# Kernel tuning notes

Hardware: AMD Instinct MI355X
Metric: run time of the kernel (lower is better)

The kernel has to match this reference:

```python
import jax, jax.numpy as jnp
import numpy as np

B = 32768
D_VIS, D_LANG, D_STATE = 256, 128, 128
D_MODEL, N_EXP, TOP_K = 512, 8, 2
D_IN = D_VIS + D_LANG + D_STATE
EPS = 1e-5

def _gelu(x):
    # torch nn.GELU default = exact erf form
    return jax.nn.gelu(x, approximate=False)

def _ln(x, g, b):
    mu = x.mean(-1, keepdims=True)
    var = ((x - mu) ** 2).mean(-1, keepdims=True)
    return (x - mu) / jnp.sqrt(var + EPS) * g + b

def setup_inputs() -> dict:
    key = jax.random.key(0)
    ks = jax.random.split(key, 16)
    f32 = jnp.float32
    def w(k, shape, fan_in):
        return jax.random.normal(k, shape, dtype=f32) * (1.0 / np.sqrt(fan_in))
    return {
        "vis":   jax.random.normal(ks[0], (B, D_VIS), dtype=f32),
        "lang":  jax.random.normal(ks[1], (B, D_LANG), dtype=f32),
        "state": jax.random.normal(ks[2], (B, D_STATE), dtype=f32),
        # fusion: Linear(D_IN, D_MODEL) + LayerNorm + GELU
        "Wf": w(ks[3], (D_IN, D_MODEL), D_IN),
        "bf": jnp.zeros((D_MODEL,), f32),
        "gf": jnp.ones((D_MODEL,), f32),
        "betaf": jnp.zeros((D_MODEL,), f32),
        # gate (bias-free); random instead of torch's zeros-init so routing is non-degenerate
        "Wg": w(ks[4], (D_MODEL, N_EXP), D_MODEL),
        # stacked expert params: d -> 2d -> d -> d, residual LayerNorm
        "W1": w(ks[5], (N_EXP, D_MODEL, 2 * D_MODEL), D_MODEL),
        "b1": jnp.zeros((N_EXP, 2 * D_MODEL), f32),
        "W2": w(ks[6], (N_EXP, 2 * D_MODEL, D_MODEL), 2 * D_MODEL),
        "b2": jnp.zeros((N_EXP, D_MODEL), f32),
        "W3": w(ks[7], (N_EXP, D_MODEL, D_MODEL), D_MODEL),
        "b3": jnp.zeros((N_EXP, D_MODEL), f32),
        "ge": jnp.ones((N_EXP, D_MODEL), f32),
        "be": jnp.zeros((N_EXP, D_MODEL), f32),
    }

def reference(vis, lang, state, Wf, bf, gf, betaf, Wg, W1, b1, W2, b2, W3, b3, ge, be):
    # fusion projection  [B, D_IN] -> [B, D_MODEL]
    x = _gelu(_ln(jnp.concatenate([vis, lang, state], axis=-1) @ Wf + bf, gf, betaf))
    logits = x @ Wg                              # [B, E]
    all_probs = jax.nn.softmax(logits, axis=-1)  # [B, E]
    top_vals, top_idx = jax.lax.top_k(logits, TOP_K)   # [B, K]
    top_w = jax.nn.softmax(top_vals, axis=-1)          # [B, K]
    # per-(token, expert) combine weight: sum_k top_w[b,k] * [top_idx[b,k]==e]
    onehot = jax.nn.one_hot(top_idx, N_EXP, dtype=x.dtype)   # [B, K, E]
    combine = (onehot * top_w[..., None]).sum(axis=1)        # [B, E]
    out = jnp.zeros_like(x)
    for e in range(N_EXP):  # small fixed expert count; dense compute, sparse combine
        h = _gelu(x @ W1[e] + b1[e])
        h = _gelu(h @ W2[e] + b2[e])
        h = h @ W3[e] + b3[e]
        y = _ln(x + h, ge[e], be[e])            # Expert: ln(x + net(x))
        out = out + combine[:, e:e + 1] * y
    # load-balancing aux loss (counts carry no gradient, as in torch scatter_add of ones)
    counts = onehot.sum(axis=(0, 1))            # [E]
    f_i = counts / (B * TOP_K)
    lb_loss = N_EXP * jnp.sum(f_i * all_probs.mean(axis=0))
    return out, lb_loss
```

## Files before the change

### kernel.cpp

```cpp
#include <hip/hip_runtime.h>
#include <math.h>

typedef __bf16     bf16x8 __attribute__((ext_vector_type(8)));
typedef _Float16   f16x8  __attribute__((ext_vector_type(8)));
typedef float      f32x4  __attribute__((ext_vector_type(4)));
typedef unsigned short u16x8 __attribute__((ext_vector_type(8)));

#define DEVI __device__ __forceinline__
constexpr int B_TOK = 32768;
constexpr int MAXT  = 520;
constexpr int NBLK  = B_TOK / 16;

DEVI unsigned short f2bf(float f){
  unsigned int u = __builtin_bit_cast(unsigned int, f);
  u += 0x7fffu + ((u >> 16) & 1u);
  return (unsigned short)(u >> 16);
}
DEVI float bf2f(unsigned short b){
  return __builtin_bit_cast(float, (unsigned int)b << 16);
}
DEVI float gelu_fast(float x){
  float z = fabsf(x) * 0.70710678118654752f;
  float t = __builtin_amdgcn_rcpf(1.f + 0.3275911f * z);
  float p = t*(0.254829592f + t*(-0.284496736f + t*(1.421413741f + t*(-1.453152027f + t*1.061405429f))));
  float e = __expf(-z * z);
  float erfz = 1.f - p * e;
  float s = copysignf(erfz, x);
  return 0.5f * x * (1.f + s);
}
DEVI void load16_lds(const void* g, void* l){
  __builtin_amdgcn_global_load_lds(
      (const __attribute__((address_space(1))) unsigned int*)g,
      (__attribute__((address_space(3))) unsigned int*)l, 16, 0, 0);
}
DEVI float wredsum(float v){
#pragma unroll
  for (int off = 32; off > 0; off >>= 1) v += __shfl_xor(v, off, 64);
  return v;
}

__global__ void transpose_cast_bf16_k(const float* __restrict__ src, unsigned short* __restrict__ dst,
                                      int R, int C){
  __shared__ float tile[32][33];
  size_t base = (size_t)blockIdx.z * R * C;
  int c0 = blockIdx.x * 32, r0 = blockIdx.y * 32;
  for (int i = threadIdx.y; i < 32; i += 8)
    tile[i][threadIdx.x] = src[base + (size_t)(r0 + i) * C + c0 + threadIdx.x];
  __syncthreads();
  for (int i = threadIdx.y; i < 32; i += 8)
    dst[base + (size_t)(c0 + i) * R + r0 + threadIdx.x] = f2bf(tile[threadIdx.x][i]);
}

__global__ void transpose_split_f16_k(const float* __restrict__ src, unsigned short* __restrict__ dh,
                                      unsigned short* __restrict__ dl, int R, int C){
  __shared__ float tile[32][33];
  int c0 = blockIdx.x * 32, r0 = blockIdx.y * 32;
  for (int i = threadIdx.y; i < 32; i += 8)
    tile[i][threadIdx.x] = src[(size_t)(r0 + i) * C + c0 + threadIdx.x];
  __syncthreads();
  for (int i = threadIdx.y; i < 32; i += 8){
    float f = tile[threadIdx.x][i];
    _Float16 h = (_Float16)f;
    _Float16 l = (_Float16)(f - (float)h);
    size_t o = (size_t)(c0 + i) * R + r0 + threadIdx.x;
    dh[o] = __builtin_bit_cast(unsigned short, h);
    dl[o] = __builtin_bit_cast(unsigned short, l);
  }
}

__global__ __launch_bounds__(256, 2) void gemm_fusion_f16split(
    const float* __restrict__ vis, const float* __restrict__ lang, const float* __restrict__ state,
    const unsigned short* __restrict__ Wh, const unsigned short* __restrict__ Wl,
    const float* __restrict__ bias, float* __restrict__ Xpre)
{
  constexpr int K = 512, N = 512;
  __shared__ alignas(16) unsigned short smemF[32768];
  unsigned short* AhS = smemF;
  unsigned short* AlS = smemF + 8192;
  unsigned short* BhS = smemF + 16384;
  unsigned short* BlS = smemF + 24576;
  const int tid = threadIdx.x;
  const int row_s = tid >> 3, col_s = (tid & 7) * 8;
  const int swz = (row_s & 7) << 3;
  const unsigned short *pbh[4], *pbl[4];
  int arow[4];
#pragma unroll
  for (int i = 0; i < 4; ++i){
    arow[i] = blockIdx.x * 128 + i * 32 + row_s;
    size_t br = (size_t)(blockIdx.y * 128 + i * 32 + row_s) * K + (col_s ^ swz);
    pbh[i] = Wh + br; pbl[i] = Wl + br;
  }
  const int w = tid >> 6, lane = tid & 63;
  const int wr = (w >> 1) * 64, wc = (w & 1) * 64;
  const int lm = lane & 15, lk8 = (lane >> 4) * 8;
  const int fxor = (lm & 7) << 3;
  f32x4 acc[4][4] = {};
  for (int k0 = 0; k0 < K; k0 += 64){
#pragma unroll
    for (int i = 0; i < 4; ++i){
      load16_lds(pbh[i] + k0, &BhS[i*2048 + tid*8]);
      load16_lds(pbl[i] + k0, &BlS[i*2048 + tid*8]);
    }
    int col = k0 + col_s;
#pragma unroll
    for (int i = 0; i < 4; ++i){
      const float* src;
      if (col < 256)      src = vis   + (size_t)arow[i] * 256 + col;
      else if (col < 384) src = lang  + (size_t)arow[i] * 128 + (col - 256);
      else                src = state + (size_t)arow[i] * 128 + (col - 384);
      float4 a = *(const float4*)src, b = *(const float4*)(src + 4);
      float f[8] = {a.x, a.y, a.z, a.w, b.x, b.y, b.z, b.w};
      u16x8 hh, ll;
#pragma unroll
      for (int j = 0; j < 8; ++j){
        _Float16 h = (_Float16)f[j];
        _Float16 l = (_Float16)(f[j] - (float)h);
        hh[j] = __builtin_bit_cast(unsigned short, h);
        ll[j] = __builtin_bit_cast(unsigned short, l);
      }
      *(u16x8*)&AhS[i*2048 + row_s*64 + (col_s ^ swz)] = hh;
      *(u16x8*)&AlS[i*2048 + row_s*64 + (col_s ^ swz)] = ll;
    }
    __syncthreads();
#pragma unroll
    for (int kk = 0; kk < 64; kk += 32){
      f16x8 fah[4], fal[4], fbh[4], fbl[4];
#pragma unroll
      for (int m = 0; m < 4; ++m){
        int ro = (wr + m*16 + lm) * 64 + ((kk + lk8) ^ fxor);
        fah[m] = *(const f16x8*)&AhS[ro];
        fal[m] = *(const f16x8*)&AlS[ro];
      }
#pragma unroll
      for (int n = 0; n < 4; ++n){
        int ro = (wc + n*16 + lm) * 64 + ((kk + lk8) ^ fxor);
        fbh[n] = *(const f16x8*)&BhS[ro];
        fbl[n] = *(const f16x8*)&BlS[ro];
      }
#pragma unroll
      for (int m = 0; m < 4; ++m)
#pragma unroll
        for (int n = 0; n < 4; ++n){
          acc[m][n] = __builtin_amdgcn_mfma_f32_16x16x32_f16(fah[m], fbh[n], acc[m][n], 0, 0, 0);
          acc[m][n] = __builtin_amdgcn_mfma_f32_16x16x32_f16(fal[m], fbh[n], acc[m][n], 0, 0, 0);
          acc[m][n] = __builtin_amdgcn_mfma_f32_16x16x32_f16(fah[m], fbl[n], acc[m][n], 0, 0, 0);
        }
    }
    __syncthreads();
  }
  float* Cs = (float*)smemF;
  const int lk4 = (lane >> 4) * 4;
#pragma unroll
  for (int n = 0; n < 4; ++n){
    float bv = bias[blockIdx.y * 128 + wc + n*16 + lm];
#pragma unroll
    for (int m = 0; m < 4; ++m)
#pragma unroll
      for (int r = 0; r < 4; ++r){
        int rr = wr + m*16 + lk4 + r;
        Cs[rr * 128 + ((wc + n*16 + lm) ^ ((rr & 7) << 2))] = acc[m][n][r] + bv;
      }
  }
  __syncthreads();
#pragma unroll
  for (int j = 0; j < 16; ++j){
    int r = j*8 + (tid >> 5), c = (tid & 31) * 4;
    float4 v = *(const float4*)&Cs[r*128 + (c ^ ((r & 7) << 2))];
    *(float4*)&Xpre[(size_t)(blockIdx.x*128 + r) * N + blockIdx.y*128 + c] = v;
  }
}

template<int K, int N, bool GATHER, bool GELU_ACT, bool GLOBAL_ROW>
__global__ __launch_bounds__(256, 2) void egemm_k(
    const unsigned short* __restrict__ A, const int* __restrict__ rowlist,
    const int* __restrict__ cnt, const int* __restrict__ nTilesP,
    const int* __restrict__ tileE, const int* __restrict__ tileR0, int chunkBase,
    const unsigned short* __restrict__ W, const float* __restrict__ bias,
    unsigned short* __restrict__ Cout)
{
  const int t = chunkBase + blockIdx.y;
  if (t >= nTilesP[0]) return;
  const int e = tileE[t], r0 = tileR0[t];
  int rows = cnt[e] - r0; rows = rows > 128 ? 128 : rows;
  __shared__ alignas(16) unsigned short smem[16384];
  unsigned short* As = smem;
  unsigned short* Bs = smem + 8192;
  const int tid = threadIdx.x;
  const int row_s = tid >> 3, col_s = (tid & 7) * 8;
  const int swz = (row_s & 7) << 3;
  const unsigned short *pa[4], *pb[4];
#pragma unroll
  for (int i = 0; i < 4; ++i){
    int ir = i * 32 + row_s;
    size_t arow;
    if (GATHER){
      int rr = ir < rows ? ir : rows - 1;
      arow = (size_t)rowlist[(size_t)e * B_TOK + r0 + rr];
    } else {
      arow = (size_t)blockIdx.y * 128 + ir;
    }
    pa[i] = A + arow * K + (col_s ^ swz);
    pb[i] = W + (size_t)e * ((size_t)N * K) + (size_t)(blockIdx.x * 128 + ir) * K + (col_s ^ swz);
  }
  const int w = tid >> 6, lane = tid & 63;
  const int wr = (w >> 1) * 64, wc = (w & 1) * 64;
  const int lm = lane & 15, lk8 = (lane >> 4) * 8;
  const int fxor = (lm & 7) << 3;
  f32x4 acc[4][4] = {};
  for (int k0 = 0; k0 < K; k0 += 64){
#pragma unroll
    for (int i = 0; i < 4; ++i) load16_lds(pa[i] + k0, &As[i*2048 + tid*8]);
#pragma unroll
    for (int i = 0; i < 4; ++i) load16_lds(pb[i] + k0, &Bs[i*2048 + tid*8]);
    __syncthreads();
#pragma unroll
    for (int kk = 0; kk < 64; kk += 32){
      bf16x8 a[4], b[4];
#pragma unroll
      for (int m = 0; m < 4; ++m)
        a[m] = *(const bf16x8*)&As[(wr + m*16 + lm)*64 + ((kk + lk8) ^ fxor)];
#pragma unroll
      for (int n = 0; n < 4; ++n)
        b[n] = *(const bf16x8*)&Bs[(wc + n*16 + lm)*64 + ((kk + lk8) ^ fxor)];
#pragma unroll
      for (int m = 0; m < 4; ++m)
#pragma unroll
        for (int n = 0; n < 4; ++n)
          acc[m][n] = __builtin_amdgcn_mfma_f32_16x16x32_bf16(a[m], b[n], acc[m][n], 0, 0, 0);
    }
    __syncthreads();
  }
  unsigned short* Cs = smem;
  const int lk4 = (lane >> 4) * 4;
#pragma unroll
  for (int n = 0; n < 4; ++n){
    float bv = bias[(size_t)e * N + blockIdx.x * 128 + wc + n*16 + lm];
#pragma unroll
    for (int m = 0; m < 4; ++m)
#pragma unroll
      for (int r = 0; r < 4; ++r){
        float v = acc[m][n][r] + bv;
        if (GELU_ACT) v = gelu_fast(v);
        int rr = wr + m*16 + lk4 + r;
        Cs[rr * 128 + ((wc + n*16 + lm) ^ ((rr & 7) << 3))] = f2bf(v);
      }
  }
  __syncthreads();
  const size_t outTile = GLOBAL_ROW ? (size_t)t * 128 : (size_t)blockIdx.y * 128;
#pragma unroll
  for (int j = 0; j < 8; ++j){
    int r = j*16 + (tid >> 4), c = (tid & 15) * 8;
    if (r < rows){
      u16x8 v = *(const u16x8*)&Cs[r*128 + (c ^ ((r & 7) << 3))];
      *(u16x8*)&Cout[(outTile + r) * N + blockIdx.x*128 + c] = v;
    }
  }
}

__global__ __launch_bounds__(256) void ln_gelu_gate_k(
    const float* __restrict__ Xpre, const float* __restrict__ gf,
    const float* __restrict__ betaf, const float* __restrict__ Wg,
    unsigned short* __restrict__ Xbf, int* __restrict__ PK,
    int* __restrict__ BlockCnt, float* __restrict__ BlockProbs)
{
  __shared__ float s_probs[8];
  __shared__ int s_cnt[8];
  __shared__ int s_pk[16];
  __shared__ float s_w[16];
  const int tid = threadIdx.x, wv = tid >> 6, lane = tid & 63;
  if (tid < 8){ s_probs[tid] = 0.f; s_cnt[tid] = 0; }
  __syncthreads();
  float gg[8], bb[8], wg[8][8];
  {
    const float4* gp = (const float4*)(gf + lane * 8);
    const float4* bp = (const float4*)(betaf + lane * 8);
    float4 g0 = gp[0], g1 = gp[1], c0 = bp[0], c1 = bp[1];
    gg[0]=g0.x; gg[1]=g0.y; gg[2]=g0.z; gg[3]=g0.w; gg[4]=g1.x; gg[5]=g1.y; gg[6]=g1.z; gg[7]=g1.w;
    bb[0]=c0.x; bb[1]=c0.y; bb[2]=c0.z; bb[3]=c0.w; bb[4]=c1.x; bb[5]=c1.y; bb[6]=c1.z; bb[7]=c1.w;
#pragma unroll
    for (int j = 0; j < 8; ++j){
      const float4* wrow = (const float4*)(Wg + (size_t)(lane * 8 + j) * 8);
      float4 w0 = wrow[0], w1 = wrow[1];
      wg[j][0]=w0.x; wg[j][1]=w0.y; wg[j][2]=w0.z; wg[j][3]=w0.w;
      wg[j][4]=w1.x; wg[j][5]=w1.y; wg[j][6]=w1.z; wg[j][7]=w1.w;
    }
  }
  float4 vv[4][2];
#pragma unroll
  for (int it = 0; it < 4; ++it){
    const int row = blockIdx.x * 16 + wv * 4 + it;
    const float* xp = Xpre + (size_t)row * 512 + lane * 8;
    vv[it][0] = *(const float4*)xp;
    vv[it][1] = *(const float4*)(xp + 4);
  }
#pragma unroll
  for (int it = 0; it < 4; ++it){
    const int tloc = wv * 4 + it;
    const int row = blockIdx.x * 16 + tloc;
    float v[8] = {vv[it][0].x, vv[it][0].y, vv[it][0].z, vv[it][0].w,
                  vv[it][1].x, vv[it][1].y, vv[it][1].z, vv[it][1].w};
    float s1 = 0.f, s2 = 0.f;
#pragma unroll
    for (int j = 0; j < 8; ++j){ s1 += v[j]; s2 += v[j]*v[j]; }
    {
      float sel = (lane & 1) ? s1 : s2;
      float r = __shfl_xor(sel, 1, 64);
      float tt = ((lane & 1) ? s2 : s1) + r;
#pragma unroll
      for (int off = 2; off < 64; off <<= 1) tt += __shfl_xor(tt, off, 64);
      float other = __shfl_xor(tt, 1, 64);
      s1 = (lane & 1) ? other : tt;
      s2 = (lane & 1) ? tt : other;
    }
    const float mu  = s1 * (1.f / 512.f);
    const float var = s2 * (1.f / 512.f) - mu * mu;
    const float inv = 1.f / sqrtf(var + 1e-5f);
    float o[8];
#pragma unroll
    for (int j = 0; j < 8; ++j)
      o[j] = gelu_fast((v[j] - mu) * inv * gg[j] + bb[j]);
    u16x8 ob;
#pragma unroll
    for (int j = 0; j < 8; ++j) ob[j] = f2bf(o[j]);
    *(u16x8*)(Xbf + (size_t)row * 512 + lane * 8) = ob;
    float acc[8] = {0.f,0.f,0.f,0.f,0.f,0.f,0.f,0.f};
#pragma unroll
    for (int j = 0; j < 8; ++j)
#pragma unroll
      for (int e = 0; e < 8; ++e) acc[e] += o[j] * wg[j][e];
    float v4[4], v2[2], v1f;
#pragma unroll
    for (int i = 0; i < 4; ++i){
      float sel = (lane & 1) ? acc[i] : acc[i+4];
      float r = __shfl_xor(sel, 1, 64);
      v4[i] = ((lane & 1) ? acc[i+4] : acc[i]) + r;
    }
#pragma unroll
    for (int i = 0; i < 2; ++i){
      float sel = (lane & 2) ? v4[i] : v4[i+2];
      float r = __shfl_xor(sel, 2, 64);
      v2[i] = ((lane & 2) ? v4[i+2] : v4[i]) + r;
    }
    {
      float sel = (lane & 4) ? v2[0] : v2[1];
      float r = __shfl_xor(sel, 4, 64);
      v1f = ((lane & 4) ? v2[1] : v2[0]) + r;
    }
#pragma unroll
    for (int off = 8; off < 64; off <<= 1) v1f += __shfl_xor(v1f, off, 64);
    float lg[8];
#pragma unroll
    for (int e = 0; e < 8; ++e){
      int src = (lane & 56) | ((e >> 2) & 1) | (((e >> 1) & 1) << 1) | ((e & 1) << 2);
      lg[e] = __shfl(v1f, src, 64);
    }
    float mx = lg[0];
#pragma unroll
    for (int e = 1; e < 8; ++e) mx = fmaxf(mx, lg[e]);
    float pe[8], ps = 0.f;
#pragma unroll
    for (int e = 0; e < 8; ++e){ pe[e] = __expf(lg[e] - mx); ps += pe[e]; }
    float invp = 1.f / ps;
    int i1 = 0;
#pragma unroll
    for (int e = 1; e < 8; ++e) if (lg[e] > lg[i1]) i1 = e;
    int i2 = (i1 == 0) ? 1 : 0;
#pragma unroll
    for (int e = 0; e < 8; ++e) if (e != i1 && lg[e] > lg[i2]) i2 = e;
    float wA = 1.f / (1.f + __expf(lg[i2] - lg[i1]));
    if (lane == 0){
#pragma unroll
      for (int e = 0; e < 8; ++e) atomicAdd(&s_probs[e], pe[e] * invp);
      int r0 = atomicAdd(&s_cnt[i1], 1);
      int r1 = atomicAdd(&s_cnt[i2], 1);
      s_pk[tloc] = i1 | (r0 << 3) | (i2 << 8) | (r1 << 16);
      s_w[tloc] = wA;
    }
  }
  __syncthreads();
  if (tid < 8){
    BlockCnt[blockIdx.x * 8 + tid] = s_cnt[tid];
    BlockProbs[blockIdx.x * 8 + tid] = s_probs[tid];
  }
  if (tid < 16){
    int t = blockIdx.x * 16 + tid;
    PK[2*t]   = s_pk[tid];
    PK[2*t+1] = __builtin_bit_cast(int, s_w[tid]);
  }
}

__global__ __launch_bounds__(256) void scan_k(
    const int* __restrict__ BlockCnt, const float* __restrict__ BlockProbs,
    int* __restrict__ BlockBase, int* __restrict__ CNT, int* __restrict__ nTiles,
    int* __restrict__ tileE, int* __restrict__ tileR0, int* __restrict__ rowBase,
    float* __restrict__ lbOut)
{
  __shared__ int sScan[256];
  __shared__ float sF[256];
  __shared__ int sTot[8];
  __shared__ float sProbTot[8];
  const int tid = threadIdx.x;
  for (int e = 0; e < 8; ++e){
    int local[8]; int sum = 0;
#pragma unroll
    for (int j = 0; j < 8; ++j){ local[j] = BlockCnt[(tid*8 + j)*8 + e]; sum += local[j]; }
    float fsum = 0.f;
#pragma unroll
    for (int j = 0; j < 8; ++j) fsum += BlockProbs[(tid*8 + j)*8 + e];
    sScan[tid] = sum; sF[tid] = fsum;
    __syncthreads();
    for (int off = 1; off < 256; off <<= 1){
      int add = (tid >= off) ? sScan[tid - off] : 0;
      __syncthreads();
      sScan[tid] += add;
      __syncthreads();
    }
    for (int off = 128; off > 0; off >>= 1){
      if (tid < off) sF[tid] += sF[tid + off];
      __syncthreads();
    }
    int base = (tid == 0) ? 0 : sScan[tid - 1];
    int run = base;
#pragma unroll
    for (int j = 0; j < 8; ++j){ BlockBase[(tid*8 + j)*8 + e] = run; run += local[j]; }
    if (tid == 0){ sTot[e] = sScan[255]; sProbTot[e] = sF[0]; }
    __syncthreads();
  }
  if (tid == 0){
    int t = 0;
    for (int e = 0; e < 8; ++e){
      int c = sTot[e]; c = c < 0 ? 0 : (c > B_TOK ? B_TOK : c);
      CNT[e] = c;
      rowBase[e] = t * 128;
      for (int r = 0; r < c; r += 128){ tileE[t] = e; tileR0[t] = r; ++t; }
    }
    nTiles[0] = t;
    for (int i = t; i < MAXT; ++i){ tileE[i] = 0; tileR0[i] = 0; }
    float acc = 0.f;
    for (int e = 0; e < 8; ++e)
      acc += ((float)sTot[e] / (float)(B_TOK * 2)) * (sProbTot[e] / (float)B_TOK);
    lbOut[0] = 8.f * acc;
  }
}

__global__ __launch_bounds__(256) void place_k(
    const int* __restrict__ PK, const int* __restrict__ BlockBase,
    int* __restrict__ rowlist, int* __restrict__ TS, float* __restrict__ TW)
{
  const int t = blockIdx.x * 256 + threadIdx.x;
  int pk = PK[2*t];
  float w0 = __builtin_bit_cast(float, PK[2*t+1]);
  int e0 = pk & 7, r0 = (pk >> 3) & 31;
  int e1 = (pk >> 8) & 7, r1 = (pk >> 16) & 31;
  int blk = t >> 4;
  int p0 = BlockBase[blk*8 + e0] + r0;
  int p1 = BlockBase[blk*8 + e1] + r1;
  rowlist[(size_t)e0 * B_TOK + p0] = t;
  rowlist[(size_t)e1 * B_TOK + p1] = t;
  TS[2*t]   = (e0 << 15) | p0;  TW[2*t]   = w0;
  TS[2*t+1] = (e1 << 15) | p1;  TW[2*t+1] = 1.f - w0;
}

__global__ __launch_bounds__(256) void combine_k(
    const unsigned short* __restrict__ Xbf, const unsigned short* __restrict__ H3F,
    const int* __restrict__ TS, const float* __restrict__ TW,
    const int* __restrict__ rowBase, const float* __restrict__ ge,
    const float* __restrict__ be, float* __restrict__ out)
{
  const int tok = blockIdx.x * 4 + (threadIdx.x >> 6);
  const int lane = threadIdx.x & 63;
  u16x8 xb = *(const u16x8*)(Xbf + (size_t)tok * 512 + lane * 8);
  float x[8];
#pragma unroll
  for (int j = 0; j < 8; ++j) x[j] = bf2f(xb[j]);
  float o[8] = {0.f,0.f,0.f,0.f,0.f,0.f,0.f,0.f};
#pragma unroll
  for (int kslot = 0; kslot < 2; ++kslot){
    int sl = TS[tok*2 + kslot];
    float wgt = TW[tok*2 + kslot];
    int e = sl >> 15, p = sl & 32767;
    size_t hrow = (size_t)(rowBase[e] + p);
    u16x8 hb = *(const u16x8*)(H3F + hrow * 512 + lane * 8);
    float s[8];
#pragma unroll
    for (int j = 0; j < 8; ++j) s[j] = x[j] + bf2f(hb[j]);
    float sm = 0.f;
#pragma unroll
    for (int j = 0; j < 8; ++j) sm += s[j];
    sm = wredsum(sm);
    float mu = sm * (1.f / 512.f);
    float q = 0.f;
#pragma unroll
    for (int j = 0; j < 8; ++j){ float d = s[j] - mu; q += d * d; }
    q = wredsum(q);
    float inv = 1.f / sqrtf(q * (1.f / 512.f) + 1e-5f);
    const float4* gp = (const float4*)(ge + (size_t)e * 512 + lane * 8);
    const float4* bp = (const float4*)(be + (size_t)e * 512 + lane * 8);
    float4 g0 = gp[0], g1 = gp[1], c0 = bp[0], c1 = bp[1];
    float gg[8] = {g0.x,g0.y,g0.z,g0.w,g1.x,g1.y,g1.z,g1.w};
    float bb[8] = {c0.x,c0.y,c0.z,c0.w,c1.x,c1.y,c1.z,c1.w};
#pragma unroll
    for (int j = 0; j < 8; ++j)
      o[j] += wgt * ((s[j]-mu)*inv*gg[j] + bb[j]);
  }
  float* op = out + (size_t)tok * 512 + lane * 8;
  *(float4*)op       = make_float4(o[0], o[1], o[2], o[3]);
  *(float4*)(op + 4) = make_float4(o[4], o[5], o[6], o[7]);
}

extern "C" void kernel_launch(void* const* d_in, const int* in_sizes, int n_in,
                              void* d_out, int out_size, void* d_ws, size_t ws_size,
                              hipStream_t stream)
{
  (void)in_sizes; (void)n_in; (void)out_size;
  const float* vis   = (const float*)d_in[0];
  const float* lang  = (const float*)d_in[1];
  const float* state = (const float*)d_in[2];
  const float* Wf    = (const float*)d_in[3];
  const float* bf    = (const float*)d_in[4];
  const float* gf    = (const float*)d_in[5];
  const float* betaf = (const float*)d_in[6];
  const float* Wg    = (const float*)d_in[7];
  const float* W1    = (const float*)d_in[8];
  const float* b1    = (const float*)d_in[9];
  const float* W2    = (const float*)d_in[10];
  const float* b2    = (const float*)d_in[11];
  const float* W3    = (const float*)d_in[12];
  const float* b3    = (const float*)d_in[13];
  const float* ge    = (const float*)d_in[14];
  const float* be    = (const float*)d_in[15];

  char* ws = (char*)d_ws;
  size_t off = 0;
  auto alloc = [&](size_t n){ size_t o = off; off += (n + 255) & ~(size_t)255; return o; };

  unsigned short* WFH  = (unsigned short*)(ws + alloc((size_t)512*512*2));
  unsigned short* WFL  = (unsigned short*)(ws + alloc((size_t)512*512*2));
  unsigned short* W1T  = (unsigned short*)(ws + alloc((size_t)8*1024*512*2));
  unsigned short* W2T  = (unsigned short*)(ws + alloc((size_t)8*512*1024*2));
  unsigned short* W3T  = (unsigned short*)(ws + alloc((size_t)8*512*512*2));
  unsigned short* XBF  = (unsigned short*)(ws + alloc((size_t)B_TOK*512*2));
  int*            RLIST= (int*)(ws + alloc((size_t)8*B_TOK*4));
  int*            TS   = (int*)(ws + alloc((size_t)B_TOK*2*4));
  float*          TW   = (float*)(ws + alloc((size_t)B_TOK*2*4));
  int*            PK   = (int*)(ws + alloc((size_t)B_TOK*2*4));
  int*            BCNT = (int*)(ws + alloc((size_t)NBLK*8*4));
  float*          BPROB= (float*)(ws + alloc((size_t)NBLK*8*4));
  int*            BBASE= (int*)(ws + alloc((size_t)NBLK*8*4));
  int*            CNT  = (int*)(ws + alloc(64));
  int*            NT   = (int*)(ws + alloc(64));
  int*            RB   = (int*)(ws + alloc(64));
  int*            TE   = (int*)(ws + alloc(MAXT*4));
  int*            TR   = (int*)(ws + alloc(MAXT*4));
  unsigned short* H3F  = (unsigned short*)(ws + alloc((size_t)MAXT*128*512*2));

  const size_t perTile = (size_t)128*1024*2 + (size_t)128*512*2;
  size_t remain = (ws_size > off) ? (ws_size - off) : 0;
  int tch, nch;
  size_t need2 = (size_t)260 * perTile, need4 = (size_t)B_TOK*512*4;
  if (remain >= need2 && need2 >= need4){ tch = 260; nch = 2; }
  else { tch = 130; nch = 4; }
  size_t regB = alloc(need2 > need4 ? (nch == 2 ? need2 : need4) : need4);
  float*          XPRE = (float*)(ws + regB);
  unsigned short* H1   = (unsigned short*)(ws + regB);
  unsigned short* H2   = H1 + (size_t)tch*128*1024;

  transpose_split_f16_k<<<dim3(16,16,1), dim3(32,8), 0, stream>>>(Wf, WFH, WFL, 512, 512);
  transpose_cast_bf16_k<<<dim3(32,16,8), dim3(32,8), 0, stream>>>(W1, W1T, 512, 1024);
  transpose_cast_bf16_k<<<dim3(16,32,8), dim3(32,8), 0, stream>>>(W2, W2T, 1024, 512);
  transpose_cast_bf16_k<<<dim3(16,16,8), dim3(32,8), 0, stream>>>(W3, W3T, 512, 512);
  gemm_fusion_f16split<<<dim3(256,4), 256, 0, stream>>>(vis, lang, state, WFH, WFL, bf, XPRE);
  ln_gelu_gate_k<<<NBLK, 256, 0, stream>>>(XPRE, gf, betaf, Wg, XBF, PK, BCNT, BPROB);
  scan_k<<<1, 256, 0, stream>>>(BCNT, BPROB, BBASE, CNT, NT, TE, TR, RB,
                                ((float*)d_out) + (size_t)B_TOK*512);
  place_k<<<B_TOK/256, 256, 0, stream>>>(PK, BBASE, RLIST, TS, TW);

  for (int c = 0; c < nch; ++c){
    int cb = c * tch;
    egemm_k<512, 1024, true,  true,  false><<<dim3(8, tch), 256, 0, stream>>>(
        XBF, RLIST, CNT, NT, TE, TR, cb, W1T, b1, H1);
    egemm_k<1024, 512, false, true,  false><<<dim3(4, tch), 256, 0, stream>>>(
        H1,  RLIST, CNT, NT, TE, TR, cb, W2T, b2, H2);
    egemm_k<512,  512, false, false, true ><<<dim3(4, tch), 256, 0, stream>>>(
        H2,  RLIST, CNT, NT, TE, TR, cb, W3T, b3, H3F);
  }
  combine_k<<<B_TOK/4, 256, 0, stream>>>(XBF, H3F, TS, TW, RB, ge, be, (float*)d_out);
}
```

Measured before the change: 546.9 us.

## Remap expert GEMM grid to XCD-grouped tiles and parallelize routing scan

The expert GEMM launches become 1D grids. Block index modulo 8 picks a contiguous group of row tiles, so that blocks landing on the same XCD (the hardware assigns workgroups round-robin across the 8 XCDs) share the A rows and expert weights in their L2. The single-block scan kernel now scans all 8 experts in one pass instead of looping serially, and fills the tile tables in parallel. The gains depend on the XCD dispatch assumption, and the padded grid adds some early-exit blocks.

```diff
diff --git a/kernel.cpp b/kernel.cpp
--- a/kernel.cpp
+++ b/kernel.cpp
@@ -170,15 +170,21 @@
   }
 }
 
-template<int K, int N, bool GATHER, bool GELU_ACT, bool GLOBAL_ROW>
+template<int K, int N, int NT, bool GATHER, bool GELU_ACT, bool GLOBAL_ROW>
 __global__ __launch_bounds__(256, 2) void egemm_k(
     const unsigned short* __restrict__ A, const int* __restrict__ rowlist,
     const int* __restrict__ cnt, const int* __restrict__ nTilesP,
-    const int* __restrict__ tileE, const int* __restrict__ tileR0, int chunkBase,
+    const int* __restrict__ tileE, const int* __restrict__ tileR0,
+    int chunkBase, int chunkTiles, int tpg,
     const unsigned short* __restrict__ W, const float* __restrict__ bias,
     unsigned short* __restrict__ Cout)
 {
-  const int t = chunkBase + blockIdx.y;
+  const int g = blockIdx.x & 7;
+  const int j = blockIdx.x >> 3;
+  const int tloc = g * tpg + j / NT;
+  const int ntile = j % NT;
+  if (tloc >= chunkTiles) return;
+  const int t = chunkBase + tloc;
   if (t >= nTilesP[0]) return;
   const int e = tileE[t], r0 = tileR0[t];
   int rows = cnt[e] - r0; rows = rows > 128 ? 128 : rows;
@@ -197,10 +203,10 @@
       int rr = ir < rows ? ir : rows - 1;
       arow = (size_t)rowlist[(size_t)e * B_TOK + r0 + rr];
     } else {
-      arow = (size_t)blockIdx.y * 128 + ir;
+      arow = (size_t)tloc * 128 + ir;
     }
     pa[i] = A + arow * K + (col_s ^ swz);
-    pb[i] = W + (size_t)e * ((size_t)N * K) + (size_t)(blockIdx.x * 128 + ir) * K + (col_s ^ swz);
+    pb[i] = W + (size_t)e * ((size_t)N * K) + (size_t)(ntile * 128 + ir) * K + (col_s ^ swz);
   }
   const int w = tid >> 6, lane = tid & 63;
   const int wr = (w >> 1) * 64, wc = (w & 1) * 64;
@@ -234,7 +240,7 @@
   const int lk4 = (lane >> 4) * 4;
 #pragma unroll
   for (int n = 0; n < 4; ++n){
-    float bv = bias[(size_t)e * N + blockIdx.x * 128 + wc + n*16 + lm];
+    float bv = bias[(size_t)e * N + ntile * 128 + wc + n*16 + lm];
 #pragma unroll
     for (int m = 0; m < 4; ++m)
 #pragma unroll
@@ -246,13 +252,13 @@
       }
   }
   __syncthreads();
-  const size_t outTile = GLOBAL_ROW ? (size_t)t * 128 : (size_t)blockIdx.y * 128;
-#pragma unroll
-  for (int j = 0; j < 8; ++j){
-    int r = j*16 + (tid >> 4), c = (tid & 15) * 8;
+  const size_t outTile = GLOBAL_ROW ? (size_t)t * 128 : (size_t)tloc * 128;
+#pragma unroll
+  for (int jj = 0; jj < 8; ++jj){
+    int r = jj*16 + (tid >> 4), c = (tid & 15) * 8;
     if (r < rows){
       u16x8 v = *(const u16x8*)&Cs[r*128 + (c ^ ((r & 7) << 3))];
-      *(u16x8*)&Cout[(outTile + r) * N + blockIdx.x*128 + c] = v;
+      *(u16x8*)&Cout[(outTile + r) * N + ntile*128 + c] = v;
     }
   }
 }
@@ -395,51 +401,77 @@
     int* __restrict__ tileE, int* __restrict__ tileR0, int* __restrict__ rowBase,
     float* __restrict__ lbOut)
 {
-  __shared__ int sScan[256];
-  __shared__ float sF[256];
+  __shared__ int sS[8][256];
+  __shared__ float sF[8][256];
   __shared__ int sTot[8];
   __shared__ float sProbTot[8];
+  __shared__ int sTileBase[9];
   const int tid = threadIdx.x;
-  for (int e = 0; e < 8; ++e){
-    int local[8]; int sum = 0;
-#pragma unroll
-    for (int j = 0; j < 8; ++j){ local[j] = BlockCnt[(tid*8 + j)*8 + e]; sum += local[j]; }
-    float fsum = 0.f;
-#pragma unroll
-    for (int j = 0; j < 8; ++j) fsum += BlockProbs[(tid*8 + j)*8 + e];
-    sScan[tid] = sum; sF[tid] = fsum;
+  int local[8][8];
+  int sum[8] = {0,0,0,0,0,0,0,0};
+  float fsum[8] = {0.f,0.f,0.f,0.f,0.f,0.f,0.f,0.f};
+#pragma unroll
+  for (int jb = 0; jb < 8; ++jb){
+    int blk = tid * 8 + jb;
+#pragma unroll
+    for (int e = 0; e < 8; ++e){
+      int c = BlockCnt[blk*8 + e];
+      local[jb][e] = c;
+      sum[e] += c;
+      fsum[e] += BlockProbs[blk*8 + e];
+    }
+  }
+#pragma unroll
+  for (int e = 0; e < 8; ++e){ sS[e][tid] = sum[e]; sF[e][tid] = fsum[e]; }
+  __syncthreads();
+  for (int off = 1; off < 256; off <<= 1){
+    int add[8];
+#pragma unroll
+    for (int e = 0; e < 8; ++e) add[e] = (tid >= off) ? sS[e][tid - off] : 0;
     __syncthreads();
-    for (int off = 1; off < 256; off <<= 1){
-      int add = (tid >= off) ? sScan[tid - off] : 0;
-      __syncthreads();
-      sScan[tid] += add;
-      __syncthreads();
-    }
-    for (int off = 128; off > 0; off >>= 1){
-      if (tid < off) sF[tid] += sF[tid + off];
-      __syncthreads();
-    }
-    int base = (tid == 0) ? 0 : sScan[tid - 1];
-    int run = base;
-#pragma unroll
-    for (int j = 0; j < 8; ++j){ BlockBase[(tid*8 + j)*8 + e] = run; run += local[j]; }
-    if (tid == 0){ sTot[e] = sScan[255]; sProbTot[e] = sF[0]; }
+#pragma unroll
+    for (int e = 0; e < 8; ++e) sS[e][tid] += add[e];
     __syncthreads();
+  }
+  for (int off = 128; off > 0; off >>= 1){
+    if (tid < off)
+#pragma unroll
+      for (int e = 0; e < 8; ++e) sF[e][tid] += sF[e][tid + off];
+    __syncthreads();
+  }
+  int base[8];
+#pragma unroll
+  for (int e = 0; e < 8; ++e) base[e] = (tid == 0) ? 0 : sS[e][tid-1];
+#pragma unroll
+  for (int jb = 0; jb < 8; ++jb){
+    int blk = tid * 8 + jb;
+#pragma unroll
+    for (int e = 0; e < 8; ++e){ BlockBase[blk*8 + e] = base[e]; base[e] += local[jb][e]; }
   }
   if (tid == 0){
     int t = 0;
+    float acc = 0.f;
     for (int e = 0; e < 8; ++e){
-      int c = sTot[e]; c = c < 0 ? 0 : (c > B_TOK ? B_TOK : c);
+      int c = sS[e][255]; c = c < 0 ? 0 : (c > B_TOK ? B_TOK : c);
+      sTot[e] = c;
       CNT[e] = c;
+      sTileBase[e] = t;
       rowBase[e] = t * 128;
-      for (int r = 0; r < c; r += 128){ tileE[t] = e; tileR0[t] = r; ++t; }
-    }
+      t += (c + 127) >> 7;
+      acc += ((float)c / (float)(B_TOK * 2)) * (sF[e][0] / (float)B_TOK);
+    }
+    sTileBase[8] = t;
     nTiles[0] = t;
-    for (int i = t; i < MAXT; ++i){ tileE[i] = 0; tileR0[i] = 0; }
-    float acc = 0.f;
-    for (int e = 0; e < 8; ++e)
-      acc += ((float)sTot[e] / (float)(B_TOK * 2)) * (sProbTot[e] / (float)B_TOK);
     lbOut[0] = 8.f * acc;
+  }
+  __syncthreads();
+  const int ntot = sTileBase[8];
+  for (int i = tid; i < MAXT; i += 256){
+    int e = 0;
+#pragma unroll
+    for (int k = 1; k <= 8; ++k) if (i >= sTileBase[k]) e = k;
+    if (i < ntot){ tileE[i] = e; tileR0[i] = (i - sTileBase[e]) * 128; }
+    else { tileE[i] = 0; tileR0[i] = 0; }
   }
 }
 
@@ -548,7 +580,7 @@
   float*          BPROB= (float*)(ws + alloc((size_t)NBLK*8*4));
   int*            BBASE= (int*)(ws + alloc((size_t)NBLK*8*4));
   int*            CNT  = (int*)(ws + alloc(64));
-  int*            NT   = (int*)(ws + alloc(64));
+  int*            NT_  = (int*)(ws + alloc(64));
   int*            RB   = (int*)(ws + alloc(64));
   int*            TE   = (int*)(ws + alloc(MAXT*4));
   int*            TR   = (int*)(ws + alloc(MAXT*4));
@@ -564,6 +596,7 @@
   float*          XPRE = (float*)(ws + regB);
   unsigned short* H1   = (unsigned short*)(ws + regB);
   unsigned short* H2   = H1 + (size_t)tch*128*1024;
+  const int tpg = (tch + 7) / 8;
 
   transpose_split_f16_k<<<dim3(16,16,1), dim3(32,8), 0, stream>>>(Wf, WFH, WFL, 512, 512);
   transpose_cast_bf16_k<<<dim3(32,16,8), dim3(32,8), 0, stream>>>(W1, W1T, 512, 1024);
@@ -571,18 +604,18 @@
   transpose_cast_bf16_k<<<dim3(16,16,8), dim3(32,8), 0, stream>>>(W3, W3T, 512, 512);
   gemm_fusion_f16split<<<dim3(256,4), 256, 0, stream>>>(vis, lang, state, WFH, WFL, bf, XPRE);
   ln_gelu_gate_k<<<NBLK, 256, 0, stream>>>(XPRE, gf, betaf, Wg, XBF, PK, BCNT, BPROB);
-  scan_k<<<1, 256, 0, stream>>>(BCNT, BPROB, BBASE, CNT, NT, TE, TR, RB,
+  scan_k<<<1, 256, 0, stream>>>(BCNT, BPROB, BBASE, CNT, NT_, TE, TR, RB,
                                 ((float*)d_out) + (size_t)B_TOK*512);
   place_k<<<B_TOK/256, 256, 0, stream>>>(PK, BBASE, RLIST, TS, TW);
 
   for (int c = 0; c < nch; ++c){
     int cb = c * tch;
-    egemm_k<512, 1024, true,  true,  false><<<dim3(8, tch), 256, 0, stream>>>(
-        XBF, RLIST, CNT, NT, TE, TR, cb, W1T, b1, H1);
-    egemm_k<1024, 512, false, true,  false><<<dim3(4, tch), 256, 0, stream>>>(
-        H1,  RLIST, CNT, NT, TE, TR, cb, W2T, b2, H2);
-    egemm_k<512,  512, false, false, true ><<<dim3(4, tch), 256, 0, stream>>>(
-        H2,  RLIST, CNT, NT, TE, TR, cb, W3T, b3, H3F);
+    egemm_k<512, 1024, 8, true,  true,  false><<<dim3(8*tpg*8), 256, 0, stream>>>(
+        XBF, RLIST, CNT, NT_, TE, TR, cb, tch, tpg, W1T, b1, H1);
+    egemm_k<1024, 512, 4, false, true,  false><<<dim3(8*tpg*4), 256, 0, stream>>>(
+        H1,  RLIST, CNT, NT_, TE, TR, cb, tch, tpg, W2T, b2, H2);
+    egemm_k<512,  512, 4, false, false, true ><<<dim3(8*tpg*4), 256, 0, stream>>>(
+        H2,  RLIST, CNT, NT_, TE, TR, cb, tch, tpg, W3T, b3, H3F);
   }
   combine_k<<<B_TOK/4, 256, 0, stream>>>(XBF, H3F, TS, TW, RB, ge, be, (float*)d_out);
 }
```

Result: faster. 470.5 us (-14.0%).
